# Optimization experiments

Measured on AMD Instinct MI355X. Metric: run time of the kernel, lower is better.

## Reference

```python
import jax, jax.numpy as jnp
import numpy as np

NUM_HEADS = 8
NUM_POINTS = 4            # sampling points per pillar point
NUM_PILLAR = 4            # points in pillar
SAMPLING_RADIUS = 0.12


def masked_softmax(logits, mask):
    # logits/mask: [B, N, H, P]; softmax over last dim, robust to fully-masked rows
    m = mask.astype(logits.dtype)
    w = jax.nn.softmax(jnp.where(mask, logits, jnp.asarray(-1e9, logits.dtype)), axis=-1) * m
    return w / jnp.clip(jnp.sum(w, axis=-1, keepdims=True), 1e-6)


def grid_sample_bilinear(feat, loc):
    # feat: [G, D, H, W]; loc: [G, Nq, P, 2] normalized to [0,1]
    # matches torch grid_sample(mode='bilinear', padding_mode='zeros', align_corners=False)
    G, D, H, W = feat.shape
    _, Nq, P, _ = loc.shape
    fm = feat.reshape(G, D, H * W).transpose(0, 2, 1)  # [G, HW, D]
    x = loc[..., 0] * W - 0.5
    y = loc[..., 1] * H - 0.5
    x0 = jnp.floor(x)
    y0 = jnp.floor(y)
    wx = x - x0
    wy = y - y0
    out = jnp.zeros((G, Nq * P, D), dtype=feat.dtype)
    corners = [(0, 0, (1 - wx) * (1 - wy)), (1, 0, wx * (1 - wy)),
               (0, 1, (1 - wx) * wy), (1, 1, wx * wy)]
    for dx, dy, w in corners:
        xi = x0 + dx
        yi = y0 + dy
        valid = (xi >= 0) & (xi < W) & (yi >= 0) & (yi < H)
        xc = jnp.clip(xi, 0, W - 1).astype(jnp.int32)
        yc = jnp.clip(yi, 0, H - 1).astype(jnp.int32)
        idx = (yc * W + xc).reshape(G, Nq * P)
        g = jnp.take_along_axis(fm, idx[:, :, None], axis=1)  # [G, Nq*P, D]
        out = out + g * (w * valid.astype(feat.dtype)).reshape(G, Nq * P, 1)
    return out.reshape(G, Nq, P, D)


def setup_inputs() -> dict:
    key = jax.random.key(0)
    ks = jax.random.split(key, 10)
    B, N, C = 1, 10000, 256
    n_cams, Himg, Wimg = 6, 60, 100
    HD = NUM_HEADS * NUM_PILLAR * NUM_POINTS  # 128
    query = jax.random.normal(ks[0], (B, N, C), jnp.float32)
    image_feats = jax.random.normal(ks[1], (B, n_cams, C, Himg, Wimg), jnp.float32)
    reference_points_cam = jax.random.uniform(ks[2], (B, n_cams, N, NUM_PILLAR, 2), jnp.float32)
    bev_mask = jax.random.bernoulli(ks[3], 0.4, (B, n_cams, N, NUM_PILLAR))
    s = 0.02
    offset_W = jax.random.normal(ks[4], (C, HD * 2), jnp.float32) * s
    offset_b = jnp.zeros((HD * 2,), jnp.float32)
    weight_W = jax.random.normal(ks[5], (C, HD), jnp.float32) * s
    weight_b = jnp.zeros((HD,), jnp.float32)
    out_W = jax.random.normal(ks[6], (C, C), jnp.float32) * s
    out_b = jnp.zeros((C,), jnp.float32)
    return {"query": query, "image_feats": image_feats,
            "reference_points_cam": reference_points_cam, "bev_mask": bev_mask,
            "offset_W": offset_W, "offset_b": offset_b,
            "weight_W": weight_W, "weight_b": weight_b,
            "out_W": out_W, "out_b": out_b}


def reference(query, image_feats, reference_points_cam, bev_mask,
              offset_W, offset_b, weight_W, weight_b, out_W, out_b):
    B, N, C = query.shape
    _, n_cams, _, Himg, Wimg = image_feats.shape
    Hh, Pp, Pn = NUM_HEADS, NUM_PILLAR, NUM_POINTS
    P = Pp * Pn
    hd = C // Hh

    offsets = jnp.tanh(query @ offset_W + offset_b) * SAMPLING_RADIUS
    offsets = offsets.reshape(B, N, Hh, Pp, Pn, 2)
    weight_logits = (query @ weight_W + weight_b).reshape(B, N, Hh, P)

    fused = jnp.zeros((B, N, C), query.dtype)
    counts = jnp.zeros((B, N), jnp.int32)
    for cam in range(n_cams):
        ref = reference_points_cam[:, cam]          # [B, N, Pp, 2]
        visible = bev_mask[:, cam]                  # [B, N, Pp]
        loc = ref[:, :, None, :, None, :] + offsets  # [B, N, H, Pp, Pn, 2]
        loc = loc.reshape(B, N, Hh, P, 2)
        vmask = jnp.broadcast_to(visible[:, :, None, :, None], (B, N, Hh, Pp, Pn)).reshape(B, N, Hh, P)
        w = masked_softmax(weight_logits, vmask)    # [B, N, H, P]
        feat = image_feats[:, cam].reshape(B * Hh, hd, Himg, Wimg)
        grid = loc.transpose(0, 2, 1, 3, 4).reshape(B * Hh, N, P, 2)
        samp = grid_sample_bilinear(feat, grid)     # [B*H, N, P, hd]
        samp = samp.reshape(B, Hh, N, P, hd).transpose(0, 2, 1, 3, 4)  # [B, N, H, P, hd]
        cam_out = jnp.sum(samp * w[..., None], axis=3).reshape(B, N, C)
        has_vis = jnp.any(visible, axis=-1)         # [B, N]
        fused = fused + cam_out * has_vis[..., None].astype(cam_out.dtype)
        counts = counts + has_vis.astype(jnp.int32)
    fused = fused / jnp.clip(counts, 1)[..., None].astype(fused.dtype)
    return fused @ out_W + out_b
```

## Files before the change

kernel.cpp:

```cpp
#include <hip/hip_runtime.h>
#include <hip/hip_bf16.h>

#define N_Q   10000
#define N_CAM 6
#define HIMG  60
#define WIMG  100
#define NPIX  6000

typedef __attribute__((ext_vector_type(4))) float f32x4;
typedef __attribute__((ext_vector_type(2))) float f32x2;
typedef __attribute__((ext_vector_type(8))) short bf16x8;

__device__ __forceinline__ unsigned short f2bf(float x) {
  __hip_bfloat16 b = __float2bfloat16(x);
  return *reinterpret_cast<unsigned short*>(&b);
}
__device__ __forceinline__ float bf2f(unsigned short u) {
  return __uint_as_float(((unsigned)u) << 16);
}
__device__ __forceinline__ float bf16lo(unsigned int u) {
  return __uint_as_float(u << 16);
}
__device__ __forceinline__ void pk_fma(f32x2& acc, f32x2 a, f32x2 b) {
  asm("v_pk_fma_f32 %0, %1, %2, %0" : "+v"(acc) : "v"(a), "v"(b));
}

#define TRANS_BLKS (N_CAM * 94)
#define QVEC_BLKS  1250

__global__ __launch_bounds__(256) void prep_trans_k(
    const float* __restrict__ in,
    const float* __restrict__ q,
    const float* __restrict__ oW, const float* __restrict__ wW,
    const float* __restrict__ outW,
    unsigned short* __restrict__ ftout,
    unsigned short* __restrict__ qh,    unsigned short* __restrict__ ql,
    unsigned short* __restrict__ oWth,  unsigned short* __restrict__ oWtl,
    unsigned short* __restrict__ wWth,  unsigned short* __restrict__ wWtl,
    unsigned short* __restrict__ outWth,unsigned short* __restrict__ outWtl) {
  __shared__ float tile[64][65];
  const int tid = threadIdx.x;
  if (blockIdx.x < TRANS_BLKS) {
    const int cam = blockIdx.x / 94;
    const int px0 = (blockIdx.x % 94) * 64;
    const int lpx = tid & 63;
    const int cg  = tid >> 6;
    const int px  = px0 + lpx;
    const bool pv = px < NPIX;

    for (int c0 = 0; c0 < 256; c0 += 64) {
#pragma unroll
      for (int i = 0; i < 16; ++i) {
        int cc = cg * 16 + i;
        tile[lpx][cc] = pv ? in[(cam * 256 + c0 + cc) * NPIX + px] : 0.f;
      }
      __syncthreads();
      const int wc = tid & 63;
      const int pg = tid >> 6;
#pragma unroll
      for (int i = 0; i < 16; ++i) {
        int lp = pg * 16 + i;
        int gpx = px0 + lp;
        if (gpx < NPIX)
          ftout[(size_t)(cam * NPIX + gpx) * 256 + c0 + wc] = f2bf(tile[lp][wc]);
      }
      __syncthreads();
    }
    return;
  }
  if (blockIdx.x < TRANS_BLKS + QVEC_BLKS) {
    const int base = ((blockIdx.x - TRANS_BLKS) * 256 + tid) * 8;
    const float4 v0 = *reinterpret_cast<const float4*>(&q[base]);
    const float4 v1 = *reinterpret_cast<const float4*>(&q[base + 4]);
    float v[8] = {v0.x, v0.y, v0.z, v0.w, v1.x, v1.y, v1.z, v1.w};
    unsigned hw[4], lw[4];
#pragma unroll
    for (int j = 0; j < 4; ++j) {
      const unsigned short h0 = f2bf(v[2 * j]),  h1 = f2bf(v[2 * j + 1]);
      const unsigned short l0 = f2bf(v[2 * j] - bf2f(h0));
      const unsigned short l1 = f2bf(v[2 * j + 1] - bf2f(h1));
      hw[j] = (unsigned)h0 | ((unsigned)h1 << 16);
      lw[j] = (unsigned)l0 | ((unsigned)l1 << 16);
    }
    uint4 vh = {hw[0], hw[1], hw[2], hw[3]};
    uint4 vl = {lw[0], lw[1], lw[2], lw[3]};
    reinterpret_cast<uint4*>(qh)[base >> 3] = vh;
    reinterpret_cast<uint4*>(ql)[base >> 3] = vl;
    return;
  }
  const int b = blockIdx.x - TRANS_BLKS - QVEC_BLKS;
  const int k = tid;
  float v; unsigned short *dh, *dl; int idx;
  if (b < 256) {
    v = oW[k * 256 + b]; dh = oWth; dl = oWtl; idx = b * 256 + k;
  } else if (b < 384) {
    int nn = b - 256; v = wW[k * 128 + nn]; dh = wWth; dl = wWtl; idx = nn * 256 + k;
  } else {
    int nn = b - 384; v = outW[k * 256 + nn]; dh = outWth; dl = outWtl; idx = nn * 256 + k;
  }
  unsigned short hv = f2bf(v);
  dh[idx] = hv;
  dl[idx] = f2bf(v - bf2f(hv));
}

__device__ __forceinline__ void gemm_body(
    const unsigned short* __restrict__ Ah, const unsigned short* __restrict__ Al,
    const unsigned short* __restrict__ Bh, const unsigned short* __restrict__ Bl,
    const float* __restrict__ bias, float* __restrict__ C,
    int M, int N, int mode, int bm, int bn, int tid) {
  const int l = tid & 63, w = tid >> 6;
  const int wm = w >> 1, wn = w & 1;
  const int lr = l & 15;
  const int lk = (l >> 4) * 8;

  const int am0 = min(bm + wm * 32 + lr, M - 1);
  const int am1 = min(bm + wm * 32 + 16 + lr, M - 1);
  const int bn0 = bn + wn * 32 + lr;
  const int bn1 = bn0 + 16;

  const bf16x8* pah0 = (const bf16x8*)(Ah + (size_t)am0 * 256 + lk);
  const bf16x8* pah1 = (const bf16x8*)(Ah + (size_t)am1 * 256 + lk);
  const bf16x8* pal0 = (const bf16x8*)(Al + (size_t)am0 * 256 + lk);
  const bf16x8* pal1 = (const bf16x8*)(Al + (size_t)am1 * 256 + lk);
  const bf16x8* pbh0 = (const bf16x8*)(Bh + (size_t)bn0 * 256 + lk);
  const bf16x8* pbh1 = (const bf16x8*)(Bh + (size_t)bn1 * 256 + lk);
  const bf16x8* pbl0 = (const bf16x8*)(Bl + (size_t)bn0 * 256 + lk);
  const bf16x8* pbl1 = (const bf16x8*)(Bl + (size_t)bn1 * 256 + lk);

  f32x4 acc00 = {}, acc01 = {}, acc10 = {}, acc11 = {};

#pragma unroll
  for (int ks = 0; ks < 8; ++ks) {
    bf16x8 ah0 = pah0[ks * 4], ah1 = pah1[ks * 4];
    bf16x8 al0 = pal0[ks * 4], al1 = pal1[ks * 4];
    bf16x8 bh0 = pbh0[ks * 4], bh1 = pbh1[ks * 4];
    bf16x8 bl0 = pbl0[ks * 4], bl1 = pbl1[ks * 4];
    acc00 = __builtin_amdgcn_mfma_f32_16x16x32_bf16(ah0, bh0, acc00, 0, 0, 0);
    acc00 = __builtin_amdgcn_mfma_f32_16x16x32_bf16(ah0, bl0, acc00, 0, 0, 0);
    acc00 = __builtin_amdgcn_mfma_f32_16x16x32_bf16(al0, bh0, acc00, 0, 0, 0);
    acc01 = __builtin_amdgcn_mfma_f32_16x16x32_bf16(ah0, bh1, acc01, 0, 0, 0);
    acc01 = __builtin_amdgcn_mfma_f32_16x16x32_bf16(ah0, bl1, acc01, 0, 0, 0);
    acc01 = __builtin_amdgcn_mfma_f32_16x16x32_bf16(al0, bh1, acc01, 0, 0, 0);
    acc10 = __builtin_amdgcn_mfma_f32_16x16x32_bf16(ah1, bh0, acc10, 0, 0, 0);
    acc10 = __builtin_amdgcn_mfma_f32_16x16x32_bf16(ah1, bl0, acc10, 0, 0, 0);
    acc10 = __builtin_amdgcn_mfma_f32_16x16x32_bf16(al1, bh0, acc10, 0, 0, 0);
    acc11 = __builtin_amdgcn_mfma_f32_16x16x32_bf16(ah1, bh1, acc11, 0, 0, 0);
    acc11 = __builtin_amdgcn_mfma_f32_16x16x32_bf16(ah1, bl1, acc11, 0, 0, 0);
    acc11 = __builtin_amdgcn_mfma_f32_16x16x32_bf16(al1, bh1, acc11, 0, 0, 0);
  }

  const float bias0 = bias[bn + wn * 32 + lr];
  const float bias1 = bias[bn + wn * 32 + 16 + lr];
  const int row0 = bm + wm * 32 + (l >> 4) * 4;
  const int col0 = bn + wn * 32 + lr;
#pragma unroll
  for (int r = 0; r < 4; ++r) {
    int rowA = row0 + r, rowB = row0 + 16 + r;
    float v00 = acc00[r] + bias0, v01 = acc01[r] + bias1;
    float v10 = acc10[r] + bias0, v11 = acc11[r] + bias1;
    if (mode == 1) {
      v00 = tanhf(v00) * 0.12f; v01 = tanhf(v01) * 0.12f;
      v10 = tanhf(v10) * 0.12f; v11 = tanhf(v11) * 0.12f;
    } else if (mode == 2) {
      v00 = __expf(v00); v01 = __expf(v01);
      v10 = __expf(v10); v11 = __expf(v11);
    }
    if (rowA < M) {
      C[(size_t)rowA * N + col0] = v00;
      C[(size_t)rowA * N + col0 + 16] = v01;
    }
    if (rowB < M) {
      C[(size_t)rowB * N + col0] = v10;
      C[(size_t)rowB * N + col0 + 16] = v11;
    }
  }
}

__global__ __launch_bounds__(256) void gemm12_k(
    const unsigned short* __restrict__ Ah, const unsigned short* __restrict__ Al,
    const unsigned short* __restrict__ B1h, const unsigned short* __restrict__ B1l,
    const float* __restrict__ b1, float* __restrict__ C1,
    const unsigned short* __restrict__ B2h, const unsigned short* __restrict__ B2l,
    const float* __restrict__ b2, float* __restrict__ C2) {
  const int by = blockIdx.x;
  if (by < 4)
    gemm_body(Ah, Al, B1h, B1l, b1, C1, N_Q, 256, 1,
              blockIdx.y * 64, by * 64, threadIdx.x);
  else
    gemm_body(Ah, Al, B2h, B2l, b2, C2, N_Q, 128, 2,
              blockIdx.y * 64, (by - 4) * 64, threadIdx.x);
}

__global__ __launch_bounds__(256) void gemm_out_k(
    const unsigned short* __restrict__ Ah, const unsigned short* __restrict__ Al,
    const unsigned short* __restrict__ Bh, const unsigned short* __restrict__ Bl,
    const float* __restrict__ bias, float* __restrict__ C) {
  gemm_body(Ah, Al, Bh, Bl, bias, C, N_Q, 256, 0,
            blockIdx.y * 64, blockIdx.x * 64, threadIdx.x);
}

__global__ __launch_bounds__(256) void sample_cam(
    const unsigned short* __restrict__ ft,
    const float* __restrict__ offs,
    const float* __restrict__ wlog,
    const float* __restrict__ refp,
    const int*   __restrict__ mask,
    float* __restrict__ partial) {
  const int tid = threadIdx.x;
  const int sub = tid >> 7;
  const int t   = tid & 127;
  const int cam = blockIdx.x / (N_Q / 2);
  const int n   = (blockIdx.x % (N_Q / 2)) * 2 + sub;
  const int h   = t >> 4;
  const int p   = t & 15;
  const int pp  = p >> 2;
  const int c   = (t >> 2) & 3;
  const int ch  = t & 3;

  const int vis = mask[(cam * N_Q + n) * 4 + pp];
  const unsigned long long bal = __ballot(vis != 0);
  if (!(bal & 0x1111ULL)) return;

  __shared__ float spt[2][1216];
  float* lds = spt[sub];
  unsigned int* ldsu = reinterpret_cast<unsigned int*>(lds);

  const float2 off = reinterpret_cast<const float2*>(offs)[n * 128 + t];
  const float E = wlog[n * 128 + t];
  const uint4* ftq2 = reinterpret_cast<const uint4*>(ft)
                      + (size_t)cam * (NPIX * 32) + (unsigned)(h * 4 + ch);

  const int abase = h * 152 + p * 9;
  const int rbase = h * 152;

  float e = vis ? E : 0.f;
  float s = e;
#pragma unroll
  for (int m = 8; m >= 1; m >>= 1)
    s += __shfl_xor(s, m, 16);
  const float wgt = e / fmaxf(s, 1e-6f);

  const float2 ref = reinterpret_cast<const float2*>(refp)[(cam * N_Q + n) * 4 + pp];
  const float x = fmaf(ref.x + off.x, (float)WIMG, -0.5f);
  const float y = fmaf(ref.y + off.y, (float)HIMG, -0.5f);
  const float x0f = floorf(x), y0f = floorf(y);
  const float wx = x - x0f, wy = y - y0f;
  const int x0 = (int)x0f, y0 = (int)y0f;
  const int x1 = x0 + 1, y1 = y0 + 1;
  const float mx0 = (x0 >= 0 && x0 < WIMG) ? 1.f : 0.f;
  const float mx1 = (x1 >= 0 && x1 < WIMG) ? 1.f : 0.f;
  const float my0 = (y0 >= 0 && y0 < HIMG) ? 1.f : 0.f;
  const float my1 = (y1 >= 0 && y1 < HIMG) ? 1.f : 0.f;
  const int xc0 = min(max(x0, 0), WIMG - 1);
  const int xc1 = min(max(x1, 0), WIMG - 1);
  const int yc0 = min(max(y0, 0), HIMG - 1);
  const int yc1 = min(max(y1, 0), HIMG - 1);
  lds[abase + 0] = (1.f - wx) * (1.f - wy) * mx0 * my0 * wgt;
  lds[abase + 1] = wx * (1.f - wy) * mx1 * my0 * wgt;
  lds[abase + 2] = (1.f - wx) * wy * mx0 * my1 * wgt;
  lds[abase + 3] = wx * wy * mx1 * my1 * wgt;
  ldsu[abase + 4] = (unsigned)(yc0 * WIMG + xc0);
  ldsu[abase + 5] = (unsigned)(yc0 * WIMG + xc1);
  ldsu[abase + 6] = (unsigned)(yc1 * WIMG + xc0);
  ldsu[abase + 7] = (unsigned)(yc1 * WIMG + xc1);
  __builtin_amdgcn_wave_barrier();

  f32x2 acc2[4] = {{0.f, 0.f}, {0.f, 0.f}, {0.f, 0.f}, {0.f, 0.f}};
  const bool pv0 = (bal      ) & 1ULL;
  const bool pv1 = (bal >>  4) & 1ULL;
  const bool pv2 = (bal >>  8) & 1ULL;
  const bool pv3 = (bal >> 12) & 1ULL;
  uint4 u0[4], u1[4], u2[4], u3[4];

#define ISSUE(U, P)                                                          \
  if (pv##P) {                                                               \
    _Pragma("unroll")                                                        \
    for (int pn = 0; pn < 4; ++pn) {                                         \
      const unsigned pix = ldsu[rbase + ((P) * 4 + pn) * 9 + 4 + c];         \
      U[pn] = ftq2[pix * 32u];                                               \
    }                                                                        \
  }
  ISSUE(u0, 0) ISSUE(u1, 1) ISSUE(u2, 2) ISSUE(u3, 3)

#define CONSUME(U, P)                                                        \
  if (pv##P) {                                                               \
    _Pragma("unroll")                                                        \
    for (int pn = 0; pn < 4; ++pn) {                                         \
      const float wv = lds[rbase + ((P) * 4 + pn) * 9 + c];                  \
      const f32x2 w2 = {wv, wv};                                             \
      f32x2 a;                                                               \
      a.x = bf16lo(U[pn].x); a.y = __uint_as_float(U[pn].x);                 \
      pk_fma(acc2[0], a, w2);                                                \
      a.x = bf16lo(U[pn].y); a.y = __uint_as_float(U[pn].y);                 \
      pk_fma(acc2[1], a, w2);                                                \
      a.x = bf16lo(U[pn].z); a.y = __uint_as_float(U[pn].z);                 \
      pk_fma(acc2[2], a, w2);                                                \
      a.x = bf16lo(U[pn].w); a.y = __uint_as_float(U[pn].w);                 \
      pk_fma(acc2[3], a, w2);                                                \
    }                                                                        \
  }
  CONSUME(u0, 0) CONSUME(u1, 1) CONSUME(u2, 2) CONSUME(u3, 3)
#undef ISSUE
#undef CONSUME

  float acc[8];
#pragma unroll
  for (int j = 0; j < 4; ++j) { acc[2 * j] = acc2[j].x; acc[2 * j + 1] = acc2[j].y; }
#pragma unroll
  for (int j = 0; j < 8; ++j) acc[j] += __shfl_xor(acc[j], 4);
#pragma unroll
  for (int j = 0; j < 8; ++j) acc[j] += __shfl_xor(acc[j], 8);

  if (c == 0) {
    float* pb = partial + ((size_t)cam * N_Q + n) * 256 + h * 32 + ch * 8;
    f32x4 a0 = {acc[0], acc[1], acc[2], acc[3]};
    f32x4 a1 = {acc[4], acc[5], acc[6], acc[7]};
    *reinterpret_cast<f32x4*>(pb)     = a0;
    *reinterpret_cast<f32x4*>(pb + 4) = a1;
  }
}

__global__ __launch_bounds__(256) void combine_k(
    const float* __restrict__ partial,
    const int*   __restrict__ mask,
    unsigned short* __restrict__ fh,
    unsigned short* __restrict__ fl) {
  const int tid  = threadIdx.x;
  const int sub  = tid >> 6;
  const int lane = tid & 63;
  const int n    = blockIdx.x * 4 + sub;

  __shared__ int sv[4][6];
  if (tid < 24) {
    const int qi = tid / 6, cam = tid - qi * 6;
    const int nn = blockIdx.x * 4 + qi;
    const int4 m4 = *reinterpret_cast<const int4*>(&mask[(cam * N_Q + nn) * 4]);
    sv[qi][cam] = (m4.x | m4.y | m4.z | m4.w) ? 1 : 0;
  }
  __syncthreads();

  f32x4 s4 = {0.f, 0.f, 0.f, 0.f};
  int cnt = 0;
#pragma unroll
  for (int cam = 0; cam < N_CAM; ++cam) {
    if (sv[sub][cam]) {
      const f32x4 v = reinterpret_cast<const f32x4*>(partial)
                          [((size_t)cam * N_Q + n) * 64 + lane];
      s4 += v; cnt++;
    }
  }
  const float inv = (cnt > 0) ? (1.f / (float)cnt) : 1.f;
  unsigned short hs[4], ls[4];
#pragma unroll
  for (int j = 0; j < 4; ++j) {
    const float v = s4[j] * inv;
    hs[j] = f2bf(v);
    ls[j] = f2bf(v - bf2f(hs[j]));
  }
  uint2 vh = {(unsigned)hs[0] | ((unsigned)hs[1] << 16),
              (unsigned)hs[2] | ((unsigned)hs[3] << 16)};
  uint2 vl = {(unsigned)ls[0] | ((unsigned)ls[1] << 16),
              (unsigned)ls[2] | ((unsigned)ls[3] << 16)};
  reinterpret_cast<uint2*>(fh)[n * 64 + lane] = vh;
  reinterpret_cast<uint2*>(fl)[n * 64 + lane] = vl;
}

extern "C" void kernel_launch(void* const* d_in, const int* in_sizes, int n_in,
                              void* d_out, int out_size, void* d_ws, size_t ws_size,
                              hipStream_t stream) {
  const float* query = (const float*)d_in[0];
  const float* feats = (const float*)d_in[1];
  const float* refp  = (const float*)d_in[2];
  const int*   mask  = (const int*)d_in[3];
  const float* oW    = (const float*)d_in[4];
  const float* ob    = (const float*)d_in[5];
  const float* wW    = (const float*)d_in[6];
  const float* wb    = (const float*)d_in[7];
  const float* outW  = (const float*)d_in[8];
  const float* outb  = (const float*)d_in[9];
  float* out = (float*)d_out;

  char* wsb = (char*)d_ws;
  size_t o = 0;
  unsigned short* ft = (unsigned short*)(wsb + o); o += (size_t)N_CAM * NPIX * 256 * 2;
  unsigned short* qh = (unsigned short*)(wsb + o); o += (size_t)N_Q * 256 * 2;
  unsigned short* ql = (unsigned short*)(wsb + o); o += (size_t)N_Q * 256 * 2;
  unsigned short* fh = (unsigned short*)(wsb + o); o += (size_t)N_Q * 256 * 2;
  unsigned short* fl = (unsigned short*)(wsb + o); o += (size_t)N_Q * 256 * 2;
  unsigned short* oWth  = (unsigned short*)(wsb + o); o += 256 * 256 * 2;
  unsigned short* oWtl  = (unsigned short*)(wsb + o); o += 256 * 256 * 2;
  unsigned short* wWth  = (unsigned short*)(wsb + o); o += 128 * 256 * 2;
  unsigned short* wWtl  = (unsigned short*)(wsb + o); o += 128 * 256 * 2;
  unsigned short* outWth = (unsigned short*)(wsb + o); o += 256 * 256 * 2;
  unsigned short* outWtl = (unsigned short*)(wsb + o); o += 256 * 256 * 2;
  float* offs    = (float*)(wsb + o); o += (size_t)N_Q * 256 * 4;
  float* wlog    = (float*)(wsb + o); o += (size_t)N_Q * 128 * 4;
  float* partial = (float*)(wsb + o); o += (size_t)N_CAM * N_Q * 256 * 4;

  prep_trans_k<<<TRANS_BLKS + QVEC_BLKS + 640, 256, 0, stream>>>(
      feats, query, oW, wW, outW, ft, qh, ql,
      oWth, oWtl, wWth, wWtl, outWth, outWtl);

  dim3 g12(6, (N_Q + 63) / 64);
  gemm12_k<<<g12, 256, 0, stream>>>(qh, ql, oWth, oWtl, ob, offs,
                                    wWth, wWtl, wb, wlog);

  sample_cam<<<N_CAM * (N_Q / 2), 256, 0, stream>>>(ft, offs, wlog, refp, mask,
                                                    partial);

  combine_k<<<N_Q / 4, 256, 0, stream>>>(partial, mask, fh, fl);

  dim3 g3(4, (N_Q + 63) / 64);
  gemm_out_k<<<g3, 256, 0, stream>>>(fh, fl, outWth, outWtl, outb, out);
}
```

Before: 167.9 us.

## Fuse query split into GEMM, merge transpose with GEMM, store partials in bf16

The query hi/lo bf16 split now happens inside the projection GEMM, which removes the separate qh/ql buffers. The image transpose and the offset/weight GEMMs share one launch, and the weight prep moves to its own small kernel. Per-camera partial sums are written as bf16 rather than fp32, halving the partial traffic between sample_cam and combine_k. The bf16 partials lose precision in the camera average, and the GEMM now re-splits A from fp32 in every block.

```diff
diff --git a/kernel.cpp b/kernel.cpp
--- a/kernel.cpp
+++ b/kernel.cpp
@@ -21,75 +21,31 @@
 __device__ __forceinline__ float bf16lo(unsigned int u) {
   return __uint_as_float(u << 16);
 }
+__device__ __forceinline__ float bf16hi(unsigned int u) {
+  return __uint_as_float(u & 0xffff0000u);
+}
 __device__ __forceinline__ void pk_fma(f32x2& acc, f32x2 a, f32x2 b) {
   asm("v_pk_fma_f32 %0, %1, %2, %0" : "+v"(acc) : "v"(a), "v"(b));
 }
-
-#define TRANS_BLKS (N_CAM * 94)
-#define QVEC_BLKS  1250
-
-__global__ __launch_bounds__(256) void prep_trans_k(
-    const float* __restrict__ in,
-    const float* __restrict__ q,
+__device__ __forceinline__ void split8(const float* pa, bf16x8& ah, bf16x8& al) {
+  const float4 v0 = *reinterpret_cast<const float4*>(pa);
+  const float4 v1 = *reinterpret_cast<const float4*>(pa + 4);
+  const float v[8] = {v0.x, v0.y, v0.z, v0.w, v1.x, v1.y, v1.z, v1.w};
+#pragma unroll
+  for (int j = 0; j < 8; ++j) {
+    const unsigned short hb = f2bf(v[j]);
+    ah[j] = (short)hb;
+    al[j] = (short)f2bf(v[j] - bf2f(hb));
+  }
+}
+
+__global__ __launch_bounds__(256) void wprep_k(
     const float* __restrict__ oW, const float* __restrict__ wW,
     const float* __restrict__ outW,
-    unsigned short* __restrict__ ftout,
-    unsigned short* __restrict__ qh,    unsigned short* __restrict__ ql,
     unsigned short* __restrict__ oWth,  unsigned short* __restrict__ oWtl,
     unsigned short* __restrict__ wWth,  unsigned short* __restrict__ wWtl,
     unsigned short* __restrict__ outWth,unsigned short* __restrict__ outWtl) {
-  __shared__ float tile[64][65];
-  const int tid = threadIdx.x;
-  if (blockIdx.x < TRANS_BLKS) {
-    const int cam = blockIdx.x / 94;
-    const int px0 = (blockIdx.x % 94) * 64;
-    const int lpx = tid & 63;
-    const int cg  = tid >> 6;
-    const int px  = px0 + lpx;
-    const bool pv = px < NPIX;
-
-    for (int c0 = 0; c0 < 256; c0 += 64) {
-#pragma unroll
-      for (int i = 0; i < 16; ++i) {
-        int cc = cg * 16 + i;
-        tile[lpx][cc] = pv ? in[(cam * 256 + c0 + cc) * NPIX + px] : 0.f;
-      }
-      __syncthreads();
-      const int wc = tid & 63;
-      const int pg = tid >> 6;
-#pragma unroll
-      for (int i = 0; i < 16; ++i) {
-        int lp = pg * 16 + i;
-        int gpx = px0 + lp;
-        if (gpx < NPIX)
-          ftout[(size_t)(cam * NPIX + gpx) * 256 + c0 + wc] = f2bf(tile[lp][wc]);
-      }
-      __syncthreads();
-    }
-    return;
-  }
-  if (blockIdx.x < TRANS_BLKS + QVEC_BLKS) {
-    const int base = ((blockIdx.x - TRANS_BLKS) * 256 + tid) * 8;
-    const float4 v0 = *reinterpret_cast<const float4*>(&q[base]);
-    const float4 v1 = *reinterpret_cast<const float4*>(&q[base + 4]);
-    float v[8] = {v0.x, v0.y, v0.z, v0.w, v1.x, v1.y, v1.z, v1.w};
-    unsigned hw[4], lw[4];
-#pragma unroll
-    for (int j = 0; j < 4; ++j) {
-      const unsigned short h0 = f2bf(v[2 * j]),  h1 = f2bf(v[2 * j + 1]);
-      const unsigned short l0 = f2bf(v[2 * j] - bf2f(h0));
-      const unsigned short l1 = f2bf(v[2 * j + 1] - bf2f(h1));
-      hw[j] = (unsigned)h0 | ((unsigned)h1 << 16);
-      lw[j] = (unsigned)l0 | ((unsigned)l1 << 16);
-    }
-    uint4 vh = {hw[0], hw[1], hw[2], hw[3]};
-    uint4 vl = {lw[0], lw[1], lw[2], lw[3]};
-    reinterpret_cast<uint4*>(qh)[base >> 3] = vh;
-    reinterpret_cast<uint4*>(ql)[base >> 3] = vl;
-    return;
-  }
-  const int b = blockIdx.x - TRANS_BLKS - QVEC_BLKS;
-  const int k = tid;
+  const int b = blockIdx.x, k = threadIdx.x;
   float v; unsigned short *dh, *dl; int idx;
   if (b < 256) {
     v = oW[k * 256 + b]; dh = oWth; dl = oWtl; idx = b * 256 + k;
@@ -103,8 +59,8 @@
   dl[idx] = f2bf(v - bf2f(hv));
 }
 
-__device__ __forceinline__ void gemm_body(
-    const unsigned short* __restrict__ Ah, const unsigned short* __restrict__ Al,
+__device__ __forceinline__ void gemm_bodyA32(
+    const float* __restrict__ A,
     const unsigned short* __restrict__ Bh, const unsigned short* __restrict__ Bl,
     const float* __restrict__ bias, float* __restrict__ C,
     int M, int N, int mode, int bm, int bn, int tid) {
@@ -118,10 +74,8 @@
   const int bn0 = bn + wn * 32 + lr;
   const int bn1 = bn0 + 16;
 
-  const bf16x8* pah0 = (const bf16x8*)(Ah + (size_t)am0 * 256 + lk);
-  const bf16x8* pah1 = (const bf16x8*)(Ah + (size_t)am1 * 256 + lk);
-  const bf16x8* pal0 = (const bf16x8*)(Al + (size_t)am0 * 256 + lk);
-  const bf16x8* pal1 = (const bf16x8*)(Al + (size_t)am1 * 256 + lk);
+  const float* pa0 = A + (size_t)am0 * 256 + lk;
+  const float* pa1 = A + (size_t)am1 * 256 + lk;
   const bf16x8* pbh0 = (const bf16x8*)(Bh + (size_t)bn0 * 256 + lk);
   const bf16x8* pbh1 = (const bf16x8*)(Bh + (size_t)bn1 * 256 + lk);
   const bf16x8* pbl0 = (const bf16x8*)(Bl + (size_t)bn0 * 256 + lk);
@@ -131,8 +85,9 @@
 
 #pragma unroll
   for (int ks = 0; ks < 8; ++ks) {
-    bf16x8 ah0 = pah0[ks * 4], ah1 = pah1[ks * 4];
-    bf16x8 al0 = pal0[ks * 4], al1 = pal1[ks * 4];
+    bf16x8 ah0, al0, ah1, al1;
+    split8(pa0 + ks * 32, ah0, al0);
+    split8(pa1 + ks * 32, ah1, al1);
     bf16x8 bh0 = pbh0[ks * 4], bh1 = pbh1[ks * 4];
     bf16x8 bl0 = pbl0[ks * 4], bl1 = pbl1[ks * 4];
     acc00 = __builtin_amdgcn_mfma_f32_16x16x32_bf16(ah0, bh0, acc00, 0, 0, 0);
@@ -176,27 +131,54 @@
   }
 }
 
-__global__ __launch_bounds__(256) void gemm12_k(
-    const unsigned short* __restrict__ Ah, const unsigned short* __restrict__ Al,
+#define TRANS_BLKS (N_CAM * 94)
+#define G12_BLKS   (157 * 6)
+
+__global__ __launch_bounds__(256) void fused_prep_gemm_k(
+    const float* __restrict__ in,
+    const float* __restrict__ q,
+    unsigned short* __restrict__ ftout,
     const unsigned short* __restrict__ B1h, const unsigned short* __restrict__ B1l,
     const float* __restrict__ b1, float* __restrict__ C1,
     const unsigned short* __restrict__ B2h, const unsigned short* __restrict__ B2l,
     const float* __restrict__ b2, float* __restrict__ C2) {
-  const int by = blockIdx.x;
-  if (by < 4)
-    gemm_body(Ah, Al, B1h, B1l, b1, C1, N_Q, 256, 1,
-              blockIdx.y * 64, by * 64, threadIdx.x);
+  __shared__ float tile[64][65];
+  const int tid = threadIdx.x;
+  if (blockIdx.x < TRANS_BLKS) {
+    const int cam = blockIdx.x / 94;
+    const int px0 = (blockIdx.x % 94) * 64;
+    const int lpx = tid & 63;
+    const int cg  = tid >> 6;
+    const int px  = px0 + lpx;
+    const bool pv = px < NPIX;
+
+    for (int c0 = 0; c0 < 256; c0 += 64) {
+#pragma unroll
+      for (int i = 0; i < 16; ++i) {
+        int cc = cg * 16 + i;
+        tile[lpx][cc] = pv ? in[(cam * 256 + c0 + cc) * NPIX + px] : 0.f;
+      }
+      __syncthreads();
+      const int wc = tid & 63;
+      const int pg = tid >> 6;
+#pragma unroll
+      for (int i = 0; i < 16; ++i) {
+        int lp = pg * 16 + i;
+        int gpx = px0 + lp;
+        if (gpx < NPIX)
+          ftout[(size_t)(cam * NPIX + gpx) * 256 + c0 + wc] = f2bf(tile[lp][wc]);
+      }
+      __syncthreads();
+    }
+    return;
+  }
+  const int b  = blockIdx.x - TRANS_BLKS;
+  const int bt = b % 6;
+  const int bm = (b / 6) * 64;
+  if (bt < 4)
+    gemm_bodyA32(q, B1h, B1l, b1, C1, N_Q, 256, 1, bm, bt * 64, tid);
   else
-    gemm_body(Ah, Al, B2h, B2l, b2, C2, N_Q, 128, 2,
-              blockIdx.y * 64, (by - 4) * 64, threadIdx.x);
-}
-
-__global__ __launch_bounds__(256) void gemm_out_k(
-    const unsigned short* __restrict__ Ah, const unsigned short* __restrict__ Al,
-    const unsigned short* __restrict__ Bh, const unsigned short* __restrict__ Bl,
-    const float* __restrict__ bias, float* __restrict__ C) {
-  gemm_body(Ah, Al, Bh, Bl, bias, C, N_Q, 256, 0,
-            blockIdx.y * 64, blockIdx.x * 64, threadIdx.x);
+    gemm_bodyA32(q, B2h, B2l, b2, C2, N_Q, 128, 2, bm, (bt - 4) * 64, tid);
 }
 
 __global__ __launch_bounds__(256) void sample_cam(
@@ -205,7 +187,7 @@
     const float* __restrict__ wlog,
     const float* __restrict__ refp,
     const int*   __restrict__ mask,
-    float* __restrict__ partial) {
+    unsigned short* __restrict__ partial) {
   const int tid = threadIdx.x;
   const int sub = tid >> 7;
   const int t   = tid & 127;
@@ -312,16 +294,17 @@
   for (int j = 0; j < 8; ++j) acc[j] += __shfl_xor(acc[j], 8);
 
   if (c == 0) {
-    float* pb = partial + ((size_t)cam * N_Q + n) * 256 + h * 32 + ch * 8;
-    f32x4 a0 = {acc[0], acc[1], acc[2], acc[3]};
-    f32x4 a1 = {acc[4], acc[5], acc[6], acc[7]};
-    *reinterpret_cast<f32x4*>(pb)     = a0;
-    *reinterpret_cast<f32x4*>(pb + 4) = a1;
+    unsigned w01 = (unsigned)f2bf(acc[0]) | ((unsigned)f2bf(acc[1]) << 16);
+    unsigned w23 = (unsigned)f2bf(acc[2]) | ((unsigned)f2bf(acc[3]) << 16);
+    unsigned w45 = (unsigned)f2bf(acc[4]) | ((unsigned)f2bf(acc[5]) << 16);
+    unsigned w67 = (unsigned)f2bf(acc[6]) | ((unsigned)f2bf(acc[7]) << 16);
+    uint4 v = {w01, w23, w45, w67};
+    reinterpret_cast<uint4*>(partial)[((size_t)cam * N_Q + n) * 32 + h * 4 + ch] = v;
   }
 }
 
 __global__ __launch_bounds__(256) void combine_k(
-    const float* __restrict__ partial,
+    const unsigned short* __restrict__ partial,
     const int*   __restrict__ mask,
     unsigned short* __restrict__ fh,
     unsigned short* __restrict__ fl) {
@@ -344,9 +327,11 @@
 #pragma unroll
   for (int cam = 0; cam < N_CAM; ++cam) {
     if (sv[sub][cam]) {
-      const f32x4 v = reinterpret_cast<const f32x4*>(partial)
+      const uint2 v = reinterpret_cast<const uint2*>(partial)
                           [((size_t)cam * N_Q + n) * 64 + lane];
-      s4 += v; cnt++;
+      s4[0] += bf16lo(v.x); s4[1] += bf16hi(v.x);
+      s4[2] += bf16lo(v.y); s4[3] += bf16hi(v.y);
+      cnt++;
     }
   }
   const float inv = (cnt > 0) ? (1.f / (float)cnt) : 1.f;
@@ -363,6 +348,72 @@
               (unsigned)ls[2] | ((unsigned)ls[3] << 16)};
   reinterpret_cast<uint2*>(fh)[n * 64 + lane] = vh;
   reinterpret_cast<uint2*>(fl)[n * 64 + lane] = vl;
+}
+
+__global__ __launch_bounds__(256) void gemm_out_k(
+    const unsigned short* __restrict__ Ah, const unsigned short* __restrict__ Al,
+    const unsigned short* __restrict__ Bh, const unsigned short* __restrict__ Bl,
+    const float* __restrict__ bias, float* __restrict__ C) {
+  const int tid = threadIdx.x;
+  const int l = tid & 63, w = tid >> 6;
+  const int wm = w >> 1, wn = w & 1;
+  const int bm = blockIdx.y * 64, bn = blockIdx.x * 64;
+  const int lr = l & 15;
+  const int lk = (l >> 4) * 8;
+  const int M = N_Q, N = 256;
+
+  const int am0 = min(bm + wm * 32 + lr, M - 1);
+  const int am1 = min(bm + wm * 32 + 16 + lr, M - 1);
+  const int bn0 = bn + wn * 32 + lr;
+  const int bn1 = bn0 + 16;
+
+  const bf16x8* pah0 = (const bf16x8*)(Ah + (size_t)am0 * 256 + lk);
+  const bf16x8* pah1 = (const bf16x8*)(Ah + (size_t)am1 * 256 + lk);
+  const bf16x8* pal0 = (const bf16x8*)(Al + (size_t)am0 * 256 + lk);
+  const bf16x8* pal1 = (const bf16x8*)(Al + (size_t)am1 * 256 + lk);
+  const bf16x8* pbh0 = (const bf16x8*)(Bh + (size_t)bn0 * 256 + lk);
+  const bf16x8* pbh1 = (const bf16x8*)(Bh + (size_t)bn1 * 256 + lk);
+  const bf16x8* pbl0 = (const bf16x8*)(Bl + (size_t)bn0 * 256 + lk);
+  const bf16x8* pbl1 = (const bf16x8*)(Bl + (size_t)bn1 * 256 + lk);
+
+  f32x4 acc00 = {}, acc01 = {}, acc10 = {}, acc11 = {};
+
+#pragma unroll
+  for (int ks = 0; ks < 8; ++ks) {
+    bf16x8 ah0 = pah0[ks * 4], ah1 = pah1[ks * 4];
+    bf16x8 al0 = pal0[ks * 4], al1 = pal1[ks * 4];
+    bf16x8 bh0 = pbh0[ks * 4], bh1 = pbh1[ks * 4];
+    bf16x8 bl0 = pbl0[ks * 4], bl1 = pbl1[ks * 4];
+    acc00 = __builtin_amdgcn_mfma_f32_16x16x32_bf16(ah0, bh0, acc00, 0, 0, 0);
+    acc00 = __builtin_amdgcn_mfma_f32_16x16x32_bf16(ah0, bl0, acc00, 0, 0, 0);
+    acc00 = __builtin_amdgcn_mfma_f32_16x16x32_bf16(al0, bh0, acc00, 0, 0, 0);
+    acc01 = __builtin_amdgcn_mfma_f32_16x16x32_bf16(ah0, bh1, acc01, 0, 0, 0);
+    acc01 = __builtin_amdgcn_mfma_f32_16x16x32_bf16(ah0, bl1, acc01, 0, 0, 0);
+    acc01 = __builtin_amdgcn_mfma_f32_16x16x32_bf16(al0, bh1, acc01, 0, 0, 0);
+    acc10 = __builtin_amdgcn_mfma_f32_16x16x32_bf16(ah1, bh0, acc10, 0, 0, 0);
+    acc10 = __builtin_amdgcn_mfma_f32_16x16x32_bf16(ah1, bl0, acc10, 0, 0, 0);
+    acc10 = __builtin_amdgcn_mfma_f32_16x16x32_bf16(al1, bh0, acc10, 0, 0, 0);
+    acc11 = __builtin_amdgcn_mfma_f32_16x16x32_bf16(ah1, bh1, acc11, 0, 0, 0);
+    acc11 = __builtin_amdgcn_mfma_f32_16x16x32_bf16(ah1, bl1, acc11, 0, 0, 0);
+    acc11 = __builtin_amdgcn_mfma_f32_16x16x32_bf16(al1, bh1, acc11, 0, 0, 0);
+  }
+
+  const float bias0 = bias[bn + wn * 32 + lr];
+  const float bias1 = bias[bn + wn * 32 + 16 + lr];
+  const int row0 = bm + wm * 32 + (l >> 4) * 4;
+  const int col0 = bn + wn * 32 + lr;
+#pragma unroll
+  for (int r = 0; r < 4; ++r) {
+    int rowA = row0 + r, rowB = row0 + 16 + r;
+    if (rowA < M) {
+      C[(size_t)rowA * N + col0] = acc00[r] + bias0;
+      C[(size_t)rowA * N + col0 + 16] = acc01[r] + bias1;
+    }
+    if (rowB < M) {
+      C[(size_t)rowB * N + col0] = acc10[r] + bias0;
+      C[(size_t)rowB * N + col0 + 16] = acc11[r] + bias1;
+    }
+  }
 }
 
 extern "C" void kernel_launch(void* const* d_in, const int* in_sizes, int n_in,
@@ -383,8 +434,6 @@
   char* wsb = (char*)d_ws;
   size_t o = 0;
   unsigned short* ft = (unsigned short*)(wsb + o); o += (size_t)N_CAM * NPIX * 256 * 2;
-  unsigned short* qh = (unsigned short*)(wsb + o); o += (size_t)N_Q * 256 * 2;
-  unsigned short* ql = (unsigned short*)(wsb + o); o += (size_t)N_Q * 256 * 2;
   unsigned short* fh = (unsigned short*)(wsb + o); o += (size_t)N_Q * 256 * 2;
   unsigned short* fl = (unsigned short*)(wsb + o); o += (size_t)N_Q * 256 * 2;
   unsigned short* oWth  = (unsigned short*)(wsb + o); o += 256 * 256 * 2;
@@ -395,15 +444,14 @@
   unsigned short* outWtl = (unsigned short*)(wsb + o); o += 256 * 256 * 2;
   float* offs    = (float*)(wsb + o); o += (size_t)N_Q * 256 * 4;
   float* wlog    = (float*)(wsb + o); o += (size_t)N_Q * 128 * 4;
-  float* partial = (float*)(wsb + o); o += (size_t)N_CAM * N_Q * 256 * 4;
-
-  prep_trans_k<<<TRANS_BLKS + QVEC_BLKS + 640, 256, 0, stream>>>(
-      feats, query, oW, wW, outW, ft, qh, ql,
-      oWth, oWtl, wWth, wWtl, outWth, outWtl);
-
-  dim3 g12(6, (N_Q + 63) / 64);
-  gemm12_k<<<g12, 256, 0, stream>>>(qh, ql, oWth, oWtl, ob, offs,
-                                    wWth, wWtl, wb, wlog);
+  unsigned short* partial = (unsigned short*)(wsb + o);
+  o += (size_t)N_CAM * N_Q * 256 * 2;
+
+  wprep_k<<<640, 256, 0, stream>>>(oW, wW, outW,
+                                   oWth, oWtl, wWth, wWtl, outWth, outWtl);
+
+  fused_prep_gemm_k<<<TRANS_BLKS + G12_BLKS, 256, 0, stream>>>(
+      feats, query, ft, oWth, oWtl, ob, offs, wWth, wWtl, wb, wlog);
 
   sample_cam<<<N_CAM * (N_Q / 2), 256, 0, stream>>>(ft, offs, wlog, refp, mask,
                                                     partial);
```

Result: faster. 151.6 us (-9.7%).
